# Kernel optimization log

Hardware: AMD Instinct MI355X
Metric: run time of the kernel (lower is better)

The kernel has to match this reference:

```python
import jax, jax.numpy as jnp
import numpy as np

N_FEATS = 32
EMBED_D = 128
BATCH = 16384
SELF_INTERACTION = False


def setup_inputs() -> dict:
    key = jax.random.key(0)
    x = jax.random.normal(key, (BATCH, N_FEATS, EMBED_D), dtype=jnp.float32)
    return {"x": x}


def reference(x):
    # x: [B, N, D] -- the stacked feature embeddings (tf.stack(inputs, axis=1))
    B, N, D = x.shape
    # dot_products: [B, N, N]
    dot = jnp.einsum('bnd,bmd->bnm', x, x)
    k = 0 if SELF_INTERACTION else 1
    iu, ju = jnp.triu_indices(N, k=k)  # upper-triangular (row-major order matches tf.boolean_mask)
    # gather pairwise interactions -> [B, N*(N-1)/2] (or N*(N+1)/2 with self-interaction)
    flat = dot[:, iu, ju]
    return flat
```

## Files before the change

### kernel.cpp

```cpp
#include <hip/hip_runtime.h>


#define WAVES_PER_BLOCK 2
#define F4_PER_BATCH 1024
#define OUT_PER_BATCH 496

__global__ __launch_bounds__(128)
void soi_gram_kernel(const float* __restrict__ x, float* __restrict__ out) {
    const int wave = threadIdx.x >> 6;
    const int lane = threadIdx.x & 63;
    const int b = blockIdx.x * WAVES_PER_BLOCK + wave;

    __shared__ float4 lds[WAVES_PER_BLOCK * F4_PER_BATCH];
    float4* myLds = &lds[wave * F4_PER_BATCH];

    const float4* xb = reinterpret_cast<const float4*>(x) + (size_t)b * F4_PER_BATCH;
    const int half = lane >> 5;
    const int c0 = lane & 31;
#pragma unroll
    for (int k = 0; k < 16; ++k) {
        const int i = 2 * k + half;
        const int src = i * 32 + (c0 ^ ((i >> 3) << 1));
        __builtin_amdgcn_global_load_lds(
            (const __attribute__((address_space(1))) void*)(xb + src),
            (__attribute__((address_space(3))) void*)(myLds + k * 64),
            16, 0, 0);
    }
    asm volatile("s_waitcnt vmcnt(0)" ::: "memory");

    const int chunk = lane & 3;
    const int tj = (lane >> 2) & 3;
    const int ti = lane >> 4;
    const int arow0 = ti << 3;
    const int brow0 = tj << 3;
    const int aswz = ti << 1;
    const int bswz = tj << 1;

    float acc[8][8];
#pragma unroll
    for (int r = 0; r < 8; ++r)
#pragma unroll
        for (int c = 0; c < 8; ++c) acc[r][c] = 0.0f;

#pragma unroll
    for (int dq = 0; dq < 8; ++dq) {
        const int d4 = chunk + (dq << 2);
        float4 a4[8], b4[8];
#pragma unroll
        for (int r = 0; r < 8; ++r)
            a4[r] = myLds[(arow0 + r) * 32 + (d4 ^ aswz)];
#pragma unroll
        for (int r = 0; r < 8; ++r)
            b4[r] = myLds[(brow0 + r) * 32 + (d4 ^ bswz)];
#pragma unroll
        for (int r = 0; r < 8; ++r)
#pragma unroll
            for (int c = 0; c < 8; ++c) {
                acc[r][c] += a4[r].x * b4[c].x;
                acc[r][c] += a4[r].y * b4[c].y;
                acc[r][c] += a4[r].z * b4[c].z;
                acc[r][c] += a4[r].w * b4[c].w;
            }
    }

#pragma unroll
    for (int r = 0; r < 8; ++r)
#pragma unroll
        for (int c = 0; c < 8; ++c) {
            float v = acc[r][c];
            v += __shfl_xor(v, 1);
            v += __shfl_xor(v, 2);
            acc[r][c] = v;
        }

    float* myLdsF = reinterpret_cast<float*>(myLds);
#pragma unroll
    for (int rr = 0; rr < 2; ++rr) {
        const int r = (chunk << 1) + rr;
        const int i = arow0 + r;
        const int base = 31 * i - (i * (i - 1)) / 2 - i - 1;
#pragma unroll
        for (int c = 0; c < 8; ++c) {
            const int j = brow0 + c;
            if (j > i) myLdsF[base + j] = acc[r][c];
        }
    }
    asm volatile("s_waitcnt lgkmcnt(0)" ::: "memory");

    const float4* packed = reinterpret_cast<const float4*>(myLdsF);
    float4* outb = reinterpret_cast<float4*>(out + (size_t)b * OUT_PER_BATCH);
    outb[lane] = packed[lane];
    if (lane < 60) outb[64 + lane] = packed[64 + lane];
}

extern "C" void kernel_launch(void* const* d_in, const int* in_sizes, int n_in,
                              void* d_out, int out_size, void* d_ws, size_t ws_size,
                              hipStream_t stream) {
    const float* x = (const float*)d_in[0];
    float* out = (float*)d_out;
    const int batch = in_sizes[0] / (32 * 128);
    const int grid = batch / WAVES_PER_BLOCK;
    soi_gram_kernel<<<grid, 128, 0, stream>>>(x, out);
}
```

Measured before the change: 434.3 us.

## Persist waves over multiple batches with double-buffered async LDS staging

Each wave now handles eight batches in a loop, using two LDS slabs. The next batch's global-to-LDS load is issued while the current batch's Gram tile is computed, so load latency overlaps with compute. The LDS repack step is gone: results are written straight to global memory as scattered scalar stores. The trade-offs are a grid eight times smaller, twice the LDS per block, and less coalesced output writes. The wait at the top of each iteration drains all outstanding memory operations, including the stores just issued, which may serialize part of the pipeline.

```diff
diff --git a/kernel.cpp b/kernel.cpp
--- a/kernel.cpp
+++ b/kernel.cpp
@@ -2,6 +2,7 @@
 
 
 #define WAVES_PER_BLOCK 2
+#define BATCHES_PER_WAVE 8
 #define F4_PER_BATCH 1024
 #define OUT_PER_BATCH 496
 
@@ -9,24 +10,29 @@
 void soi_gram_kernel(const float* __restrict__ x, float* __restrict__ out) {
     const int wave = threadIdx.x >> 6;
     const int lane = threadIdx.x & 63;
-    const int b = blockIdx.x * WAVES_PER_BLOCK + wave;
 
-    __shared__ float4 lds[WAVES_PER_BLOCK * F4_PER_BATCH];
-    float4* myLds = &lds[wave * F4_PER_BATCH];
+    __shared__ float4 lds[WAVES_PER_BLOCK * 2 * F4_PER_BATCH];
+    float4* slab0 = &lds[(wave * 2 + 0) * F4_PER_BATCH];
+    float4* slab1 = &lds[(wave * 2 + 1) * F4_PER_BATCH];
 
-    const float4* xb = reinterpret_cast<const float4*>(x) + (size_t)b * F4_PER_BATCH;
+    const long bBase =
+        ((long)blockIdx.x * WAVES_PER_BLOCK + wave) * BATCHES_PER_WAVE;
+
     const int half = lane >> 5;
     const int c0 = lane & 31;
+
+    auto stage = [&](float4* dst, long b) {
+        const float4* xb = reinterpret_cast<const float4*>(x) + b * F4_PER_BATCH;
 #pragma unroll
-    for (int k = 0; k < 16; ++k) {
-        const int i = 2 * k + half;
-        const int src = i * 32 + (c0 ^ ((i >> 3) << 1));
-        __builtin_amdgcn_global_load_lds(
-            (const __attribute__((address_space(1))) void*)(xb + src),
-            (__attribute__((address_space(3))) void*)(myLds + k * 64),
-            16, 0, 0);
-    }
-    asm volatile("s_waitcnt vmcnt(0)" ::: "memory");
+        for (int k = 0; k < 16; ++k) {
+            const int i = 2 * k + half;
+            const int src = i * 32 + (c0 ^ ((i >> 3) << 1));
+            __builtin_amdgcn_global_load_lds(
+                (const __attribute__((address_space(1))) void*)(xb + src),
+                (__attribute__((address_space(3))) void*)(dst + k * 64),
+                16, 0, 0);
+        }
+    };
 
     const int chunk = lane & 3;
     const int tj = (lane >> 2) & 3;
@@ -36,61 +42,66 @@
     const int aswz = ti << 1;
     const int bswz = tj << 1;
 
-    float acc[8][8];
+    stage(slab0, bBase);
+
+#pragma unroll 1
+    for (int t = 0; t < BATCHES_PER_WAVE; ++t) {
+        asm volatile("s_waitcnt vmcnt(0) lgkmcnt(0)" ::: "memory");
+
+        float4* cur = (t & 1) ? slab1 : slab0;
+        float4* nxt = (t & 1) ? slab0 : slab1;
+        if (t + 1 < BATCHES_PER_WAVE) stage(nxt, bBase + t + 1);
+
+        float acc[8][8];
 #pragma unroll
-    for (int r = 0; r < 8; ++r)
+        for (int r = 0; r < 8; ++r)
 #pragma unroll
-        for (int c = 0; c < 8; ++c) acc[r][c] = 0.0f;
+            for (int c = 0; c < 8; ++c) acc[r][c] = 0.0f;
 
 #pragma unroll
-    for (int dq = 0; dq < 8; ++dq) {
-        const int d4 = chunk + (dq << 2);
-        float4 a4[8], b4[8];
+        for (int dq = 0; dq < 8; ++dq) {
+            const int d4 = chunk + (dq << 2);
+            float4 a4[8], b4[8];
 #pragma unroll
-        for (int r = 0; r < 8; ++r)
-            a4[r] = myLds[(arow0 + r) * 32 + (d4 ^ aswz)];
+            for (int r = 0; r < 8; ++r)
+                a4[r] = cur[(arow0 + r) * 32 + (d4 ^ aswz)];
 #pragma unroll
-        for (int r = 0; r < 8; ++r)
-            b4[r] = myLds[(brow0 + r) * 32 + (d4 ^ bswz)];
+            for (int r = 0; r < 8; ++r)
+                b4[r] = cur[(brow0 + r) * 32 + (d4 ^ bswz)];
+#pragma unroll
+            for (int r = 0; r < 8; ++r)
+#pragma unroll
+                for (int c = 0; c < 8; ++c) {
+                    acc[r][c] += a4[r].x * b4[c].x;
+                    acc[r][c] += a4[r].y * b4[c].y;
+                    acc[r][c] += a4[r].z * b4[c].z;
+                    acc[r][c] += a4[r].w * b4[c].w;
+                }
+        }
+
 #pragma unroll
         for (int r = 0; r < 8; ++r)
 #pragma unroll
             for (int c = 0; c < 8; ++c) {
-                acc[r][c] += a4[r].x * b4[c].x;
-                acc[r][c] += a4[r].y * b4[c].y;
-                acc[r][c] += a4[r].z * b4[c].z;
-                acc[r][c] += a4[r].w * b4[c].w;
+                float v = acc[r][c];
+                v += __shfl_xor(v, 1);
+                v += __shfl_xor(v, 2);
+                acc[r][c] = v;
             }
-    }
 
+        float* outb = out + (size_t)(bBase + t) * OUT_PER_BATCH;
 #pragma unroll
-    for (int r = 0; r < 8; ++r)
+        for (int rr = 0; rr < 2; ++rr) {
+            const int r = (chunk << 1) + rr;
+            const int i = arow0 + r;
+            const int base = 31 * i - (i * (i - 1)) / 2 - i - 1;
 #pragma unroll
-        for (int c = 0; c < 8; ++c) {
-            float v = acc[r][c];
-            v += __shfl_xor(v, 1);
-            v += __shfl_xor(v, 2);
-            acc[r][c] = v;
-        }
-
-    float* myLdsF = reinterpret_cast<float*>(myLds);
-#pragma unroll
-    for (int rr = 0; rr < 2; ++rr) {
-        const int r = (chunk << 1) + rr;
-        const int i = arow0 + r;
-        const int base = 31 * i - (i * (i - 1)) / 2 - i - 1;
-#pragma unroll
-        for (int c = 0; c < 8; ++c) {
-            const int j = brow0 + c;
-            if (j > i) myLdsF[base + j] = acc[r][c];
+            for (int c = 0; c < 8; ++c) {
+                const int j = brow0 + c;
+                if (j > i) outb[base + j] = acc[r][c];
+            }
         }
     }
-    asm volatile("s_waitcnt lgkmcnt(0)" ::: "memory");
-
-    const float4* packed = reinterpret_cast<const float4*>(myLdsF);
-    float4* outb = reinterpret_cast<float4*>(out + (size_t)b * OUT_PER_BATCH);
-    outb[lane] = packed[lane];
-    if (lane < 60) outb[64 + lane] = packed[64 + lane];
 }
 
 extern "C" void kernel_launch(void* const* d_in, const int* in_sizes, int n_in,
@@ -99,6 +110,6 @@
     const float* x = (const float*)d_in[0];
     float* out = (float*)d_out;
     const int batch = in_sizes[0] / (32 * 128);
-    const int grid = batch / WAVES_PER_BLOCK;
+    const int grid = batch / (WAVES_PER_BLOCK * BATCHES_PER_WAVE);
     soi_gram_kernel<<<grid, 128, 0, stream>>>(x, out);
 }
```

New measurement: 488.3 us. +12.4%, slower.
